# Optimization experiments

Measured on AMD Instinct MI355X. Metric: run time of the kernel, lower is better.

## Reference

```python
import jax, jax.numpy as jnp
import numpy as np

B, T, C = 4, 512, 1024          # batch, seq, n_embd
E, H = 8, 2048                  # n_total_experts, ffn hidden (ffn_factor*C)
N_SHARED, K = 1, 2              # shared experts, top-k routed
ROUTE_SCALE = 1.0


def setup_inputs() -> dict:
    key = jax.random.key(0)
    ks = jax.random.split(key, 6)
    s = 0.02
    return {
        "x": jax.random.normal(ks[0], (B, T, C), jnp.float32),
        "gate_w": jax.random.normal(ks[1], (C, E), jnp.float32) * s,
        "gate_b": jnp.zeros((E,), jnp.float32),
        "w1": jax.random.normal(ks[2], (E, C, H), jnp.float32) * s,
        "b1": jnp.zeros((E, H), jnp.float32),
        "w2": jax.random.normal(ks[3], (E, H, C), jnp.float32) * s,
        "b2": jnp.zeros((E, C), jnp.float32),
        "w3": jax.random.normal(ks[4], (E, C, H), jnp.float32) * s,
        "b3": jnp.zeros((E, H), jnp.float32),
    }


def reference(x, gate_w, gate_b, w1, b1, w2, b2, w3, b3):
    Bs, Ts, Cs = x.shape
    N = Bs * Ts
    xf = x.reshape(N, Cs)

    # --- gating (softmax in fp32, as in the torch code) ---
    logits = xf @ gate_w + gate_b                       # [N, E]
    scores = jax.nn.softmax(logits.astype(jnp.float32), axis=-1).astype(logits.dtype)

    topk_vals, topk_idx = jax.lax.top_k(scores[:, N_SHARED:], K)   # routed experts
    shared_ix = jnp.broadcast_to(jnp.arange(N_SHARED), (N, N_SHARED))
    all_idx = jnp.concatenate([shared_ix, topk_idx + N_SHARED], axis=-1)  # [N, S+K]
    all_w = jnp.concatenate([scores[:, :N_SHARED], topk_vals], axis=-1) * ROUTE_SCALE

    # combine-weight matrix: each expert selected at most once per token
    rows = jnp.arange(N)[:, None]
    cw = jnp.zeros((N, E), x.dtype).at[rows, all_idx].add(all_w)  # [N, E]

    # --- per-expert SwiGLU MLP (vectorized over experts; zero cw masks out) ---
    a = jnp.einsum('nc,ech->neh', xf, w1) + b1          # [N, E, H]
    g = jnp.einsum('nc,ech->neh', xf, w3) + b3
    h = jax.nn.silu(g) * a
    out = jnp.einsum('neh,ehc,ne->nc', h, w2, cw) + cw @ b2  # weighted combine

    # --- balance loss ---
    flat_idx = all_idx.reshape(-1)
    usage = jnp.zeros((E,), jnp.float32).at[flat_idx].add(1.0)
    score_sum = jnp.zeros((E,), jnp.float32).at[flat_idx].add(all_w.reshape(-1).astype(jnp.float32))
    Kp = float(N_SHARED + K)
    bal_loss = jnp.sum((float(E) / (Kp * N)) * usage * (score_sum / N))

    return out.reshape(Bs, Ts, Cs), bal_loss
```

## Files before the change

kernel.cpp:

```cpp
#include <hip/hip_runtime.h>
#include <stdint.h>

#define N_TOK 2048
#define C_DIM 1024
#define H_DIM 2048
#define NE 8
#define NSLOT 3

#define BM 128
#define BN 128
#define BK 64
#define PGRID 1024

#define WS_COUNTS   0
#define WS_PLAN     256
#define WS_CW       (WS_PLAN + 1024)
#define WS_ROUTE    (WS_CW + N_TOK*NE*4)
#define WS_LISTS    (WS_ROUTE + N_TOK*4)
#define WS_XB       (WS_LISTS + NE*N_TOK*4)
#define WS_HBUF     (WS_XB + (size_t)N_TOK*C_DIM*2)
#define WS_OUTSLOT  (WS_HBUF + (size_t)N_TOK*NSLOT*H_DIM*2)
#define WS_WT1T     (WS_OUTSLOT + (size_t)N_TOK*NSLOT*C_DIM*2)
#define WS_WT3T     (WS_WT1T + (size_t)NE*H_DIM*C_DIM*2)
#define WS_WT2T     (WS_WT3T + (size_t)NE*H_DIM*C_DIM*2)

typedef short bf16x8 __attribute__((ext_vector_type(8)));
typedef float f32x4 __attribute__((ext_vector_type(4)));

union FragU { bf16x8 v; uint2 u2[2]; };

__device__ __forceinline__ unsigned short f2b(float f) {
    union { float f; uint32_t u; } v; v.f = f;
    return (unsigned short)((v.u + 0x7fffu + ((v.u >> 16) & 1u)) >> 16);
}
__device__ __forceinline__ float b2f(unsigned short s) {
    union { uint32_t u; float f; } v; v.u = ((uint32_t)s) << 16; return v.f;
}

__device__ __forceinline__ void gload16(const unsigned short* g, unsigned short* l) {
    __builtin_amdgcn_global_load_lds(
        (const __attribute__((address_space(1))) unsigned int*)g,
        (__attribute__((address_space(3))) unsigned int*)l, 16, 0, 0);
}

__device__ __forceinline__ void tcast256(
        const float* __restrict__ src, unsigned short* __restrict__ dtile0,
        int N, int NKT, int kt, int nBase, char* lb, int t) {
    uint32_t* L = (uint32_t*)lb;
    const int l = t & 63, w = t >> 6;
    const float* s = src + (size_t)(kt * 64) * N + nBase;
#pragma unroll 4
    for (int i = 0; i < 16; i++) {
        int k = w * 16 + i;
        float4 v = *(const float4*)(s + (size_t)k * N + 4 * l);
        uint2 p;
        p.x = (uint32_t)f2b(v.x) | ((uint32_t)f2b(v.y) << 16);
        p.y = (uint32_t)f2b(v.z) | ((uint32_t)f2b(v.w) << 16);
        *(uint2*)(L + k * 130 + 2 * l) = p;
    }
    __syncthreads();
    const int rn = t >> 3, cc = t & 7;
#pragma unroll
    for (int s2 = 0; s2 < 8; s2++) {
        int n = s2 * 32 + rn;
        int np = n >> 1, hi = (n & 1) * 16;
        uint32_t o[4];
#pragma unroll
        for (int u = 0; u < 4; u++) {
            uint32_t a = L[(cc * 8 + 2 * u) * 130 + np];
            uint32_t b = L[(cc * 8 + 2 * u + 1) * 130 + np];
            o[u] = ((a >> hi) & 0xffffu) | (((b >> hi) & 0xffffu) << 16);
        }
        unsigned short* drow = dtile0 + (size_t)s2 * NKT * 2048 + rn * 64 + cc * 8;
        *(uint4*)drow = *(uint4*)o;
    }
}

__global__ __launch_bounds__(256) void prep_kernel(
        const float* __restrict__ x, const float* __restrict__ gw,
        const float* __restrict__ gb, const float* __restrict__ w1,
        const float* __restrict__ w3, const float* __restrict__ w2,
        float* __restrict__ cw, unsigned short* __restrict__ xb,
        int* __restrict__ route, unsigned short* __restrict__ wt1t,
        unsigned short* __restrict__ wt3t, unsigned short* __restrict__ wt2t) {
    __shared__ __align__(16) char smem[33792];
    const int b = blockIdx.x;
    if (b >= 2560) {
        int bb = b - 2560;
        int e = bb >> 7, rem = bb & 127, kt = rem >> 2, nB = rem & 3;
        tcast256(w2 + (size_t)e * H_DIM * C_DIM,
                 wt2t + ((size_t)(e * 32 + nB * 8) * 32 + kt) * 2048,
                 C_DIM, 32, kt, nB * 256, smem, threadIdx.x);
        return;
    }
    if (b >= 512) {
        int bb = b - 512;
        int op = bb >> 10, r2 = bb & 1023;
        int e = r2 >> 7, rem = r2 & 127, kt = rem >> 3, nB = rem & 7;
        const float* src = (op ? w3 : w1) + (size_t)e * C_DIM * H_DIM;
        unsigned short* dst = (op ? wt3t : wt1t) +
                              ((size_t)(e * 64 + nB * 8) * 16 + kt) * 2048;
        tcast256(src, dst, H_DIM, 16, kt, nB * 256, smem, threadIdx.x);
        return;
    }
    int n = (b * 256 + threadIdx.x) >> 6;
    int lane = threadIdx.x & 63;
    float acc[NE];
#pragma unroll
    for (int e = 0; e < NE; e++) acc[e] = 0.f;
    for (int c = lane; c < C_DIM; c += 64) {
        float xv = x[n * C_DIM + c];
        xb[n * C_DIM + c] = f2b(xv);
        const float* g = gw + c * NE;
#pragma unroll
        for (int e = 0; e < NE; e++) acc[e] += xv * g[e];
    }
#pragma unroll
    for (int e = 0; e < NE; e++) {
#pragma unroll
        for (int off = 32; off >= 1; off >>= 1) acc[e] += __shfl_xor(acc[e], off, 64);
        acc[e] += gb[e];
    }
    float m = acc[0];
#pragma unroll
    for (int e = 1; e < NE; e++) m = fmaxf(m, acc[e]);
    float s = 0.f, sc[NE];
#pragma unroll
    for (int e = 0; e < NE; e++) { sc[e] = __expf(acc[e] - m); s += sc[e]; }
    float inv = 1.f / s;
#pragma unroll
    for (int e = 0; e < NE; e++) sc[e] *= inv;
    int i1 = 1; float v1 = sc[1];
#pragma unroll
    for (int e = 2; e < NE; e++) if (sc[e] > v1) { v1 = sc[e]; i1 = e; }
    int i2 = 0; float v2 = -1.f;
#pragma unroll
    for (int e = 1; e < NE; e++) if (e != i1 && sc[e] > v2) { v2 = sc[e]; i2 = e; }
    if (lane < NE) {
        float v = 0.f;
        if (lane == 0) v = sc[0];
        else if (lane == i1) v = v1;
        else if (lane == i2) v = v2;
        cw[n * NE + lane] = v;
    }
    if (lane == 0) route[n] = i1 | (i2 << 8);
}

__global__ void lists_kernel(const int* __restrict__ route, int* __restrict__ counts,
                             int* __restrict__ lists) {
    const int e = blockIdx.x, lane = threadIdx.x;
    if (e == 0) {
        for (int base = 0; base < N_TOK; base += 64)
            lists[base + lane] = (base + lane) * 4;
        if (lane == 0) counts[0] = N_TOK;
        return;
    }
    int cnt = 0;
    for (int base = 0; base < N_TOK; base += 64) {
        int r = route[base + lane];
        int i1 = r & 255, i2 = (r >> 8) & 255;
        bool mt = (i1 == e) || (i2 == e);
        int slot = (i1 == e) ? 1 : 2;
        unsigned long long mask = __ballot(mt);
        int pos = __popcll(mask & ((1ull << lane) - 1ull));
        if (mt) lists[e * N_TOK + cnt + pos] = (base + lane) * 4 + slot;
        cnt += __popcll(mask);
    }
    if (lane == 0) counts[e] = cnt;
}

__global__ void plan_kernel(const int* __restrict__ counts, int* __restrict__ plan) {
    if (threadIdx.x == 0) {
        int p = 0;
        for (int e = 0; e < NE; e++) {
            int nb = (counts[e] + BM - 1) / BM;
            for (int m = 0; m < nb; m++) plan[1 + p++] = (e << 8) | m;
        }
        plan[0] = p;
    }
}

#define STAGE(aoff, boff) do {                                            \
    _Pragma("unroll")                                                     \
    for (int i_ = 0; i_ < 4; i_++)                                        \
        gload16(asrc[i_] + (aoff), As + (i_ * 256 + t) * 8);              \
    _Pragma("unroll")                                                     \
    for (int i_ = 0; i_ < 4; i_++)                                        \
        gload16(bsrc[i_] + (boff), Bs + (i_ * 256 + t) * 8);              \
} while (0)

#define COMPUTE() do {                                                    \
    __builtin_amdgcn_s_setprio(1);                                        \
    _Pragma("unroll")                                                     \
    for (int j_ = 0; j_ < 2; j_++) {                                      \
        FragU af[4], bf[4];                                               \
        _Pragma("unroll")                                                 \
        for (int mt = 0; mt < 4; mt++) {                                  \
            int row = wr * 64 + mt * 16 + ln15;                           \
            int slot = (j_ * 4 + lg) ^ swz;                               \
            af[mt].v = *(const bf16x8*)(As + row * BK + slot * 8);        \
        }                                                                 \
        _Pragma("unroll")                                                 \
        for (int nt = 0; nt < 4; nt++) {                                  \
            int row = wc * 64 + nt * 16 + ln15;                           \
            int slot = (j_ * 4 + lg) ^ swz;                               \
            bf[nt].v = *(const bf16x8*)(Bs + row * BK + slot * 8);        \
        }                                                                 \
        _Pragma("unroll")                                                 \
        for (int mt = 0; mt < 4; mt++)                                    \
            _Pragma("unroll")                                             \
            for (int nt = 0; nt < 4; nt++)                                \
                acc[mt][nt] = __builtin_amdgcn_mfma_f32_16x16x32_bf16(    \
                    af[mt].v, bf[nt].v, acc[mt][nt], 0, 0, 0);            \
    }                                                                     \
    __builtin_amdgcn_s_setprio(0);                                        \
} while (0)

#define KLOOP(NK) do {                                                    \
    for (int kt = 0; kt < (NK); kt++) {                                   \
        STAGE(kt * BK, kt * 2048);                                        \
        asm volatile("s_waitcnt vmcnt(0)" ::: "memory");                  \
        __builtin_amdgcn_s_barrier();                                     \
        COMPUTE();                                                        \
        __builtin_amdgcn_s_barrier();                                     \
    }                                                                     \
} while (0)

__global__ __launch_bounds__(256, 4) void expert_up_kernel(
        const unsigned short* __restrict__ xb, const unsigned short* __restrict__ wt1t,
        const unsigned short* __restrict__ wt3t, const float* __restrict__ b1,
        const float* __restrict__ b3, const int* __restrict__ counts,
        const int* __restrict__ lists, const int* __restrict__ plan,
        unsigned short* __restrict__ hbuf) {
    const int t = threadIdx.x;
    const int lane = t & 63, w = t >> 6;
    const int ln15 = lane & 15, lg = lane >> 4;
    const int wr = w >> 1, wc = w & 1;
    const int swz = ln15 & 7;

    __shared__ __align__(16) unsigned short As[BM * BK];
    __shared__ __align__(16) unsigned short Bs[BN * BK];
    __shared__ int rowtok[BM];

    const int ntile = plan[0] << 5;
    for (int tile = blockIdx.x; tile < ntile; tile += PGRID) {
        const int mi = tile >> 5, nb = tile & 31;
        const int ent = plan[1 + mi];
        const int e = ent >> 8, m0 = (ent & 255) * BM;
        const int cnt = counts[e];

        if (t < BM) {
            int r = m0 + t;
            rowtok[t] = lists[e * N_TOK + (r < cnt ? r : cnt - 1)];
        }
        __syncthreads();

        const unsigned short* asrc[4];
        const unsigned short* bsrc[4];
#pragma unroll
        for (int i = 0; i < 4; i++) {
            int c = i * 256 + t;
            int row = c >> 3, kc = (c & 7) ^ (row & 7);
            asrc[i] = xb + (size_t)(rowtok[row] >> 2) * C_DIM + kc * 8;
        }
#pragma unroll
        for (int i = 0; i < 4; i++) {
            int c = i * 256 + t;
            int r = c >> 3, kc = (c & 7) ^ (r & 7);
            int g = r >> 4;
            const unsigned short* wb = (g & 1) ? wt3t : wt1t;
            int rb = nb * 2 + (g >> 2);
            int trow = ((g >> 1) & 1) * 16 + (r & 15);
            bsrc[i] = wb + ((size_t)(e * 64 + rb) * 16) * 2048 + trow * 64 + kc * 8;
        }

        f32x4 acc[4][4];
#pragma unroll
        for (int a = 0; a < 4; a++)
#pragma unroll
            for (int b = 0; b < 4; b++) acc[a][b] = (f32x4){0.f, 0.f, 0.f, 0.f};

        KLOOP(C_DIM / BK);

#pragma unroll
        for (int p = 0; p < 2; p++) {
            int h = nb * 64 + (wc * 2 + p) * 16 + ln15;
            float bb1 = b1[e * H_DIM + h], bb3 = b3[e * H_DIM + h];
#pragma unroll
            for (int mt = 0; mt < 4; mt++) {
#pragma unroll
                for (int jj = 0; jj < 4; jj++) {
                    int mrow = wr * 64 + mt * 16 + lg * 4 + jj;
                    float av = acc[mt][2 * p][jj] + bb1;
                    float gv = acc[mt][2 * p + 1][jj] + bb3;
                    float hv = av * gv / (1.f + __expf(-gv));
                    int ent2 = rowtok[mrow];
                    hbuf[(size_t)((ent2 >> 2) * NSLOT + (ent2 & 3)) * H_DIM + h] = f2b(hv);
                }
            }
        }
        __syncthreads();
    }
}

__global__ __launch_bounds__(256, 4) void expert_down_kernel(
        const unsigned short* __restrict__ hbuf, const unsigned short* __restrict__ wt2t,
        const float* __restrict__ b2, const float* __restrict__ cw,
        const int* __restrict__ counts, const int* __restrict__ lists,
        const int* __restrict__ plan, unsigned short* __restrict__ outslot) {
    const int t = threadIdx.x;
    const int lane = t & 63, w = t >> 6;
    const int ln15 = lane & 15, lg = lane >> 4;
    const int wr = w >> 1, wc = w & 1;
    const int swz = ln15 & 7;

    __shared__ __align__(16) unsigned short As[BM * BK];
    __shared__ __align__(16) unsigned short Bs[BN * BK];
    __shared__ int rowtok[BM];

    const int ntile = plan[0] << 3;
    for (int tile = blockIdx.x; tile < ntile; tile += PGRID) {
        const int mi = tile >> 3, nb = tile & 7;
        const int ent = plan[1 + mi];
        const int e = ent >> 8, m0 = (ent & 255) * BM;
        const int cnt = counts[e];
        const int c0 = nb * BN;

        if (t < BM) {
            int r = m0 + t;
            rowtok[t] = lists[e * N_TOK + (r < cnt ? r : cnt - 1)];
        }
        __syncthreads();

        const unsigned short* asrc[4];
        const unsigned short* bsrc[4];
#pragma unroll
        for (int i = 0; i < 4; i++) {
            int c = i * 256 + t;
            int row = c >> 3, kc = (c & 7) ^ (row & 7);
            int ent2 = rowtok[row];
            asrc[i] = hbuf + (size_t)((ent2 >> 2) * NSLOT + (ent2 & 3)) * H_DIM + kc * 8;
        }
#pragma unroll
        for (int i = 0; i < 4; i++) {
            int c = i * 256 + t;
            int r = c >> 3, kc = (c & 7) ^ (r & 7);
            int rb = nb * 4 + (r >> 5);
            bsrc[i] = wt2t + ((size_t)(e * 32 + rb) * 32) * 2048 +
                      (size_t)(r & 31) * 64 + kc * 8;
        }

        f32x4 acc[4][4];
#pragma unroll
        for (int a = 0; a < 4; a++)
#pragma unroll
            for (int b = 0; b < 4; b++) acc[a][b] = (f32x4){0.f, 0.f, 0.f, 0.f};

        KLOOP(H_DIM / BK);

#pragma unroll
        for (int nt = 0; nt < 4; nt++) {
            int col = c0 + wc * 64 + nt * 16 + ln15;
            float bb = b2[e * C_DIM + col];
#pragma unroll
            for (int mt = 0; mt < 4; mt++) {
#pragma unroll
                for (int jj = 0; jj < 4; jj++) {
                    int mrow = wr * 64 + mt * 16 + lg * 4 + jj;
                    int ent2 = rowtok[mrow];
                    int tok = ent2 >> 2, slot = ent2 & 3;
                    float cwv = cw[tok * NE + e];
                    outslot[(size_t)(tok * NSLOT + slot) * C_DIM + col] =
                        f2b(cwv * (acc[mt][nt][jj] + bb));
                }
            }
        }
        __syncthreads();
    }
}

__global__ __launch_bounds__(256) void reduce_loss_kernel(
        const unsigned short* __restrict__ os, const float* __restrict__ cw,
        const int* __restrict__ counts, float* __restrict__ out) {
    if (blockIdx.x < 1024) {
        int i = blockIdx.x * 256 + threadIdx.x;
        int n = i >> 7;
        int c = (i & 127) * 8;
        const unsigned short* p0 = os + ((size_t)n * NSLOT + 0) * C_DIM + c;
        const unsigned short* p1 = os + ((size_t)n * NSLOT + 1) * C_DIM + c;
        const unsigned short* p2 = os + ((size_t)n * NSLOT + 2) * C_DIM + c;
        uint4 a = *(const uint4*)p0, b = *(const uint4*)p1, d = *(const uint4*)p2;
        const unsigned short* sa = (const unsigned short*)&a;
        const unsigned short* sb = (const unsigned short*)&b;
        const unsigned short* sd = (const unsigned short*)&d;
        float r[8];
#pragma unroll
        for (int j = 0; j < 8; j++) r[j] = b2f(sa[j]) + b2f(sb[j]) + b2f(sd[j]);
        float* o = out + (size_t)n * C_DIM + c;
        *(float4*)o = *(float4*)&r[0];
        *(float4*)(o + 4) = *(float4*)&r[4];
    } else if (threadIdx.x < 64) {
        int lane = threadIdx.x;
        float ss[NE];
#pragma unroll
        for (int e = 0; e < NE; e++) ss[e] = 0.f;
        for (int n = lane; n < N_TOK; n += 64) {
#pragma unroll
            for (int e = 0; e < NE; e++) ss[e] += cw[n * NE + e];
        }
#pragma unroll
        for (int e = 0; e < NE; e++) {
#pragma unroll
            for (int off = 32; off >= 1; off >>= 1) ss[e] += __shfl_xor(ss[e], off, 64);
        }
        if (lane == 0) {
            float bal = 0.f;
            const float fac = (float)NE / (3.f * (float)N_TOK * (float)N_TOK);
#pragma unroll
            for (int e = 0; e < NE; e++) bal += fac * (float)counts[e] * ss[e];
            out[(size_t)N_TOK * C_DIM] = bal;
        }
    }
}

extern "C" void kernel_launch(void* const* d_in, const int* in_sizes, int n_in,
                              void* d_out, int out_size, void* d_ws, size_t ws_size,
                              hipStream_t stream) {
    const float* x  = (const float*)d_in[0];
    const float* gw = (const float*)d_in[1];
    const float* gb = (const float*)d_in[2];
    const float* w1 = (const float*)d_in[3];
    const float* b1 = (const float*)d_in[4];
    const float* w2 = (const float*)d_in[5];
    const float* b2 = (const float*)d_in[6];
    const float* w3 = (const float*)d_in[7];
    const float* b3 = (const float*)d_in[8];
    float* out = (float*)d_out;
    char* ws = (char*)d_ws;
    int*            counts = (int*)(ws + WS_COUNTS);
    int*            plan   = (int*)(ws + WS_PLAN);
    float*          cw     = (float*)(ws + WS_CW);
    int*            route  = (int*)(ws + WS_ROUTE);
    int*            lists  = (int*)(ws + WS_LISTS);
    unsigned short* xb     = (unsigned short*)(ws + WS_XB);
    unsigned short* hbuf   = (unsigned short*)(ws + WS_HBUF);
    unsigned short* oslot  = (unsigned short*)(ws + WS_OUTSLOT);
    unsigned short* wt1t   = (unsigned short*)(ws + WS_WT1T);
    unsigned short* wt3t   = (unsigned short*)(ws + WS_WT3T);
    unsigned short* wt2t   = (unsigned short*)(ws + WS_WT2T);

    hipLaunchKernelGGL(prep_kernel, dim3(3584), dim3(256), 0, stream,
                       x, gw, gb, w1, w3, w2, cw, xb, route, wt1t, wt3t, wt2t);
    hipLaunchKernelGGL(lists_kernel, dim3(NE), dim3(64), 0, stream,
                       route, counts, lists);
    hipLaunchKernelGGL(plan_kernel, dim3(1), dim3(64), 0, stream, counts, plan);
    hipLaunchKernelGGL(expert_up_kernel, dim3(PGRID), dim3(256), 0, stream,
                       xb, wt1t, wt3t, b1, b3, counts, lists, plan, hbuf);
    hipLaunchKernelGGL(expert_down_kernel, dim3(PGRID), dim3(256), 0, stream,
                       hbuf, wt2t, b2, cw, counts, lists, plan, oslot);
    hipLaunchKernelGGL(reduce_loss_kernel, dim3(1025), dim3(256), 0, stream,
                       oslot, cw, counts, out);
}
```

Before: 195.5 us.

## Move w2 transpose-cast into up-projection kernel tail and narrow down-proj N tile

The w2 fp32-to-bf16 transpose-cast moves out of the prep kernel and into the tail of the expert up-projection kernel, so that work overlaps with up-GEMM tiles that finish unevenly instead of lengthening prep. The down-projection kernel drops its N tile from 128 to 64, giving twice as many tiles to fill the 1024-block persistent grid, at the cost of less B-tile reuse per A load. The up kernel now uses a shared char smem buffer for both the GEMM and the cast.

```diff
diff --git a/kernel.cpp b/kernel.cpp
--- a/kernel.cpp
+++ b/kernel.cpp
@@ -79,20 +79,11 @@
 __global__ __launch_bounds__(256) void prep_kernel(
         const float* __restrict__ x, const float* __restrict__ gw,
         const float* __restrict__ gb, const float* __restrict__ w1,
-        const float* __restrict__ w3, const float* __restrict__ w2,
-        float* __restrict__ cw, unsigned short* __restrict__ xb,
-        int* __restrict__ route, unsigned short* __restrict__ wt1t,
-        unsigned short* __restrict__ wt3t, unsigned short* __restrict__ wt2t) {
+        const float* __restrict__ w3, float* __restrict__ cw,
+        unsigned short* __restrict__ xb, int* __restrict__ route,
+        unsigned short* __restrict__ wt1t, unsigned short* __restrict__ wt3t) {
     __shared__ __align__(16) char smem[33792];
     const int b = blockIdx.x;
-    if (b >= 2560) {
-        int bb = b - 2560;
-        int e = bb >> 7, rem = bb & 127, kt = rem >> 2, nB = rem & 3;
-        tcast256(w2 + (size_t)e * H_DIM * C_DIM,
-                 wt2t + ((size_t)(e * 32 + nB * 8) * 32 + kt) * 2048,
-                 C_DIM, 32, kt, nB * 256, smem, threadIdx.x);
-        return;
-    }
     if (b >= 512) {
         int bb = b - 512;
         int op = bb >> 10, r2 = bb & 1023;
@@ -180,20 +171,20 @@
     }
 }
 
-#define STAGE(aoff, boff) do {                                            \
+#define STAGE(NA, NB, aoff, boff) do {                                    \
     _Pragma("unroll")                                                     \
-    for (int i_ = 0; i_ < 4; i_++)                                        \
+    for (int i_ = 0; i_ < (NA); i_++)                                     \
         gload16(asrc[i_] + (aoff), As + (i_ * 256 + t) * 8);              \
     _Pragma("unroll")                                                     \
-    for (int i_ = 0; i_ < 4; i_++)                                        \
+    for (int i_ = 0; i_ < (NB); i_++)                                     \
         gload16(bsrc[i_] + (boff), Bs + (i_ * 256 + t) * 8);              \
 } while (0)
 
-#define COMPUTE() do {                                                    \
+#define COMPUTE(NT, BEXPR) do {                                           \
     __builtin_amdgcn_s_setprio(1);                                        \
     _Pragma("unroll")                                                     \
     for (int j_ = 0; j_ < 2; j_++) {                                      \
-        FragU af[4], bf[4];                                               \
+        FragU af[4], bf[NT];                                              \
         _Pragma("unroll")                                                 \
         for (int mt = 0; mt < 4; mt++) {                                  \
             int row = wr * 64 + mt * 16 + ln15;                           \
@@ -201,27 +192,27 @@
             af[mt].v = *(const bf16x8*)(As + row * BK + slot * 8);        \
         }                                                                 \
         _Pragma("unroll")                                                 \
-        for (int nt = 0; nt < 4; nt++) {                                  \
-            int row = wc * 64 + nt * 16 + ln15;                           \
+        for (int nt = 0; nt < (NT); nt++) {                               \
+            int row = (BEXPR);                                            \
             int slot = (j_ * 4 + lg) ^ swz;                               \
             bf[nt].v = *(const bf16x8*)(Bs + row * BK + slot * 8);        \
         }                                                                 \
         _Pragma("unroll")                                                 \
         for (int mt = 0; mt < 4; mt++)                                    \
             _Pragma("unroll")                                             \
-            for (int nt = 0; nt < 4; nt++)                                \
+            for (int nt = 0; nt < (NT); nt++)                             \
                 acc[mt][nt] = __builtin_amdgcn_mfma_f32_16x16x32_bf16(    \
                     af[mt].v, bf[nt].v, acc[mt][nt], 0, 0, 0);            \
     }                                                                     \
     __builtin_amdgcn_s_setprio(0);                                        \
 } while (0)
 
-#define KLOOP(NK) do {                                                    \
+#define KLOOP(NK, NA, NB, NT, BEXPR) do {                                 \
     for (int kt = 0; kt < (NK); kt++) {                                   \
-        STAGE(kt * BK, kt * 2048);                                        \
+        STAGE(NA, NB, kt * BK, kt * 2048);                                \
         asm volatile("s_waitcnt vmcnt(0)" ::: "memory");                  \
         __builtin_amdgcn_s_barrier();                                     \
-        COMPUTE();                                                        \
+        COMPUTE(NT, BEXPR);                                               \
         __builtin_amdgcn_s_barrier();                                     \
     }                                                                     \
 } while (0)
@@ -231,16 +222,18 @@
         const unsigned short* __restrict__ wt3t, const float* __restrict__ b1,
         const float* __restrict__ b3, const int* __restrict__ counts,
         const int* __restrict__ lists, const int* __restrict__ plan,
-        unsigned short* __restrict__ hbuf) {
+        unsigned short* __restrict__ hbuf, const float* __restrict__ w2,
+        unsigned short* __restrict__ wt2t) {
     const int t = threadIdx.x;
     const int lane = t & 63, w = t >> 6;
     const int ln15 = lane & 15, lg = lane >> 4;
     const int wr = w >> 1, wc = w & 1;
     const int swz = ln15 & 7;
 
-    __shared__ __align__(16) unsigned short As[BM * BK];
-    __shared__ __align__(16) unsigned short Bs[BN * BK];
-    __shared__ int rowtok[BM];
+    __shared__ __align__(16) char smem[33792];
+    unsigned short* As = (unsigned short*)smem;
+    unsigned short* Bs = (unsigned short*)(smem + BM * BK * 2);
+    int* rowtok = (int*)(smem + BM * BK * 2 + BN * BK * 2);
 
     const int ntile = plan[0] << 5;
     for (int tile = blockIdx.x; tile < ntile; tile += PGRID) {
@@ -280,7 +273,7 @@
 #pragma unroll
             for (int b = 0; b < 4; b++) acc[a][b] = (f32x4){0.f, 0.f, 0.f, 0.f};
 
-        KLOOP(C_DIM / BK);
+        KLOOP(C_DIM / BK, 4, 4, 4, wc * 64 + nt * 16 + ln15);
 
 #pragma unroll
         for (int p = 0; p < 2; p++) {
@@ -300,6 +293,14 @@
             }
         }
         __syncthreads();
+    }
+
+    {
+        int bb = blockIdx.x;
+        int e = bb >> 7, rem = bb & 127, kt = rem >> 2, nB = rem & 3;
+        tcast256(w2 + (size_t)e * H_DIM * C_DIM,
+                 wt2t + ((size_t)(e * 32 + nB * 8) * 32 + kt) * 2048,
+                 C_DIM, 32, kt, nB * 256, smem, t);
     }
 }
 
@@ -315,16 +316,16 @@
     const int swz = ln15 & 7;
 
     __shared__ __align__(16) unsigned short As[BM * BK];
-    __shared__ __align__(16) unsigned short Bs[BN * BK];
+    __shared__ __align__(16) unsigned short Bs[64 * BK];
     __shared__ int rowtok[BM];
 
-    const int ntile = plan[0] << 3;
+    const int ntile = plan[0] << 4;
     for (int tile = blockIdx.x; tile < ntile; tile += PGRID) {
-        const int mi = tile >> 3, nb = tile & 7;
+        const int mi = tile >> 4, nb = tile & 15;
         const int ent = plan[1 + mi];
         const int e = ent >> 8, m0 = (ent & 255) * BM;
         const int cnt = counts[e];
-        const int c0 = nb * BN;
+        const int c0 = nb * 64;
 
         if (t < BM) {
             int r = m0 + t;
@@ -333,7 +334,7 @@
         __syncthreads();
 
         const unsigned short* asrc[4];
-        const unsigned short* bsrc[4];
+        const unsigned short* bsrc[2];
 #pragma unroll
         for (int i = 0; i < 4; i++) {
             int c = i * 256 + t;
@@ -342,25 +343,24 @@
             asrc[i] = hbuf + (size_t)((ent2 >> 2) * NSLOT + (ent2 & 3)) * H_DIM + kc * 8;
         }
 #pragma unroll
-        for (int i = 0; i < 4; i++) {
+        for (int i = 0; i < 2; i++) {
             int c = i * 256 + t;
-            int r = c >> 3, kc = (c & 7) ^ (r & 7);
-            int rb = nb * 4 + (r >> 5);
-            bsrc[i] = wt2t + ((size_t)(e * 32 + rb) * 32) * 2048 +
-                      (size_t)(r & 31) * 64 + kc * 8;
-        }
-
-        f32x4 acc[4][4];
+            int row = c >> 3, kc = (c & 7) ^ (row & 7);
+            bsrc[i] = wt2t + (size_t)(e * 32 + nb * 2 + (row >> 5)) * 32 * 2048 +
+                      (size_t)(row & 31) * 64 + kc * 8;
+        }
+
+        f32x4 acc[4][2];
 #pragma unroll
         for (int a = 0; a < 4; a++)
 #pragma unroll
-            for (int b = 0; b < 4; b++) acc[a][b] = (f32x4){0.f, 0.f, 0.f, 0.f};
-
-        KLOOP(H_DIM / BK);
-
-#pragma unroll
-        for (int nt = 0; nt < 4; nt++) {
-            int col = c0 + wc * 64 + nt * 16 + ln15;
+            for (int b = 0; b < 2; b++) acc[a][b] = (f32x4){0.f, 0.f, 0.f, 0.f};
+
+        KLOOP(H_DIM / BK, 4, 2, 2, wc * 32 + nt * 16 + ln15);
+
+#pragma unroll
+        for (int nt = 0; nt < 2; nt++) {
+            int col = c0 + wc * 32 + nt * 16 + ln15;
             float bb = b2[e * C_DIM + col];
 #pragma unroll
             for (int mt = 0; mt < 4; mt++) {
@@ -449,13 +449,13 @@
     unsigned short* wt3t   = (unsigned short*)(ws + WS_WT3T);
     unsigned short* wt2t   = (unsigned short*)(ws + WS_WT2T);
 
-    hipLaunchKernelGGL(prep_kernel, dim3(3584), dim3(256), 0, stream,
-                       x, gw, gb, w1, w3, w2, cw, xb, route, wt1t, wt3t, wt2t);
+    hipLaunchKernelGGL(prep_kernel, dim3(2560), dim3(256), 0, stream,
+                       x, gw, gb, w1, w3, cw, xb, route, wt1t, wt3t);
     hipLaunchKernelGGL(lists_kernel, dim3(NE), dim3(64), 0, stream,
                        route, counts, lists);
     hipLaunchKernelGGL(plan_kernel, dim3(1), dim3(64), 0, stream, counts, plan);
     hipLaunchKernelGGL(expert_up_kernel, dim3(PGRID), dim3(256), 0, stream,
-                       xb, wt1t, wt3t, b1, b3, counts, lists, plan, hbuf);
+                       xb, wt1t, wt3t, b1, b3, counts, lists, plan, hbuf, w2, wt2t);
     hipLaunchKernelGGL(expert_down_kernel, dim3(PGRID), dim3(256), 0, stream,
                        hbuf, wt2t, b2, cw, counts, lists, plan, oslot);
     hipLaunchKernelGGL(reduce_loss_kernel, dim3(1025), dim3(256), 0, stream,
```

New measurement: 196.3 us. Within noise of the previous version (+0.4%).
